# Optimization experiments

Hardware: AMD Instinct MI355X
Metric: run time of the kernel (lower is better)

The kernel has to match this reference:

```python
import jax, jax.numpy as jnp
import numpy as np

THRESHOLD = 0.5
NEG_POS = 3
ALPHA = 1.0


def cxcy_to_xy(b):
    return jnp.concatenate([b[:, :2] - b[:, 2:] / 2, b[:, :2] + b[:, 2:] / 2], axis=-1)


def xy_to_cxcy(b):
    return jnp.concatenate([(b[:, :2] + b[:, 2:]) / 2, b[:, 2:] - b[:, :2]], axis=-1)


def encode_bboxes(cxcy, priors_cxcy):
    # standard SSD encoding with variances (0.1, 0.2)
    g_cxcy = (cxcy[:, :2] - priors_cxcy[:, :2]) / (priors_cxcy[:, 2:] / 10.0)
    g_wh = jnp.log(cxcy[:, 2:] / priors_cxcy[:, 2:]) * 5.0
    return jnp.concatenate([g_cxcy, g_wh], axis=-1)


def compute_iou(a, b):
    # a: [n,4] xyxy, b: [m,4] xyxy -> [n,m]
    lt = jnp.maximum(a[:, None, :2], b[None, :, :2])
    rb = jnp.minimum(a[:, None, 2:], b[None, :, 2:])
    wh = jnp.clip(rb - lt, 0.0)
    inter = wh[..., 0] * wh[..., 1]
    area_a = (a[:, 2] - a[:, 0]) * (a[:, 3] - a[:, 1])
    area_b = (b[:, 2] - b[:, 0]) * (b[:, 3] - b[:, 1])
    return inter / (area_a[:, None] + area_b[None, :] - inter)


def setup_inputs() -> dict:
    key = jax.random.key(0)
    k1, k2, k3, k4, k5, k6 = jax.random.split(key, 6)
    B, D, C, O = 128, 8732, 21, 16
    loc_pred = jax.random.normal(k1, (B, D, 4), dtype=jnp.float32)
    cls_pred = jax.random.normal(k2, (B, D, C), dtype=jnp.float32)
    # valid gt boxes: xmin<xmax, ymin<ymax
    p = jax.random.uniform(k3, (B, O, 4), dtype=jnp.float32)
    x1 = jnp.minimum(p[..., 0], p[..., 2])
    x2 = jnp.maximum(p[..., 0], p[..., 2]) + 1e-2
    y1 = jnp.minimum(p[..., 1], p[..., 3])
    y2 = jnp.maximum(p[..., 1], p[..., 3]) + 1e-2
    gt_boxes = jnp.stack([x1, y1, x2, y2], axis=-1)
    gt_labels = jax.random.randint(k4, (B, O), 1, C)
    # priors in cxcywh, w/h in (0.05, 0.5)
    cxy = jax.random.uniform(k5, (D, 2), dtype=jnp.float32)
    wh = jax.random.uniform(k6, (D, 2), dtype=jnp.float32) * 0.45 + 0.05
    default_boxes = jnp.concatenate([cxy, wh], axis=-1)
    return {"loc_pred": loc_pred, "cls_pred": cls_pred, "gt_boxes": gt_boxes,
            "gt_labels": gt_labels, "default_boxes": default_boxes}


def _match_and_losses(loc_pred, cls_pred, gt_boxes, gt_labels, default_boxes):
    B, D, C = cls_pred.shape
    O = gt_boxes.shape[1]
    db_xy = cxcy_to_xy(default_boxes)

    def match_one(boxes_i, labels_i):
        iou = compute_iou(boxes_i, db_xy)                 # [O, D]
        best_truth_overlap = iou.max(axis=0)              # [D]
        best_truth_idx = iou.argmax(axis=0)               # [D]
        best_default_idx = iou.argmax(axis=1)             # [O]
        best_truth_idx = best_truth_idx.at[best_default_idx].set(jnp.arange(O))
        best_truth_overlap = best_truth_overlap.at[best_default_idx].set(1.0)
        labels = labels_i[best_truth_idx]                 # [D]
        labels = jnp.where(best_truth_overlap < THRESHOLD, 0, labels)
        matched_xy = boxes_i[best_truth_idx]              # [D,4]
        loc = encode_bboxes(xy_to_cxcy(matched_xy), default_boxes)
        return loc, labels

    loc_t, conf_t = jax.vmap(match_one)(gt_boxes, gt_labels)  # [B,D,4], [B,D]
    loc_t = jax.lax.stop_gradient(loc_t)  # targets carry no grad (requires_grad=False)

    pos = conf_t > 0                                      # [B,D]
    n_positive = pos.sum(axis=1)                          # [B]
    n_pos_total = n_positive.sum()

    # SmoothL1 (beta=1), mean over positive elements (num_pos * 4)
    diff = loc_pred - loc_t
    ad = jnp.abs(diff)
    sl1 = jnp.where(ad < 1.0, 0.5 * diff * diff, ad - 0.5)
    loc_loss = (sl1 * pos[..., None]).sum() / (n_pos_total.astype(jnp.float32) * 4.0)

    # per-element cross entropy
    logp = jax.nn.log_softmax(cls_pred, axis=-1)          # [B,D,C]
    ce = -jnp.take_along_axis(logp, conf_t[..., None], axis=-1)[..., 0]  # [B,D]

    conf_pos_sum = (ce * pos).sum()
    neg_loss = jnp.where(pos, 0.0, ce)
    neg_sorted = -jnp.sort(-neg_loss, axis=1)             # descending per row
    ranks = jnp.arange(D)[None, :]
    hard = ranks < (NEG_POS * n_positive)[:, None]
    conf_neg_sum = (neg_sorted * hard).sum()
    conf_loss = (conf_neg_sum + conf_pos_sum) / n_pos_total.astype(jnp.float32)

    return ALPHA * loc_loss + conf_loss


def reference(loc_pred, cls_pred, gt_boxes, gt_labels, default_boxes):
    return _match_and_losses(loc_pred, cls_pred, gt_boxes, gt_labels, default_boxes)
```

## Files before the change

kernel.cpp:

```cpp
#include <hip/hip_runtime.h>

#define BB 128
#define DD 8732
#define OO 16
#define CC 21
#define NG2 4366
#define NBLK_C 18
#define NLB (BB * NBLK_C)
#define NV 35

typedef float f32x2 __attribute__((ext_vector_type(2)));

__device__ __forceinline__ float smoothl1(float d) {
    float ad = fabsf(d);
    return (ad < 1.0f) ? 0.5f * d * d : ad - 0.5f;
}

__global__ __launch_bounds__(256) void fused_all(
    const float4* __restrict__ loc_pred,
    const float*  __restrict__ cls,
    const float4* __restrict__ gt_boxes,
    const int*    __restrict__ gt_labels,
    const float4* __restrict__ db,
    unsigned long long* __restrict__ partial,
    float* __restrict__ ce_neg,
    float* __restrict__ part_sl1,
    int*   __restrict__ part_np,
    float* __restrict__ part_ce)
{
    const int b = blockIdx.y, jb = blockIdx.x, tid = threadIdx.x;
    const int g = jb * 256 + tid;
    __shared__ float s_ax1[OO], s_ay1[OO], s_ax2[OO], s_ay2[OO], s_area[OO];
    __shared__ int   s_lab[OO];
    __shared__ unsigned long long s_keys[8][257];
    __shared__ float s_f[8];
    __shared__ int   s_i[4];

    if (tid < OO) {
        float4 gg = gt_boxes[b * OO + tid];
        s_ax1[tid] = gg.x; s_ay1[tid] = gg.y; s_ax2[tid] = gg.z; s_ay2[tid] = gg.w;
        s_area[tid] = (gg.z - gg.x) * (gg.w - gg.y);
        s_lab[tid] = gt_labels[b * OO + tid];
    }
    __syncthreads();

    unsigned long long key[OO];
    #pragma unroll
    for (int o = 0; o < OO; ++o) key[o] = 0ull;
    int lab_r[2] = {0, 0};
    int bi_r[2]  = {0, 0};

    const int row0 = g * 2;
    if (g < NG2) {
        #pragma unroll
        for (int r = 0; r < 2; ++r) {
            const int d = row0 + r;
            float4 p = db[d];
            float px1 = p.x - p.z * 0.5f, py1 = p.y - p.w * 0.5f;
            float px2 = p.x + p.z * 0.5f, py2 = p.y + p.w * 0.5f;
            float area_b = (px2 - px1) * (py2 - py1);
            unsigned dl = (unsigned)(DD - 1 - d);
            float best = -1.0f; int bi = 0;
            #pragma unroll
            for (int o = 0; o < OO; ++o) {
                float w = fmaxf(fminf(s_ax2[o], px2) - fmaxf(s_ax1[o], px1), 0.0f);
                float h = fmaxf(fminf(s_ay2[o], py2) - fmaxf(s_ay1[o], py1), 0.0f);
                float inter = w * h;
                float uni = s_area[o] + area_b - inter;
                float iou = inter * __builtin_amdgcn_rcpf(uni);
                unsigned long long kk = ((unsigned long long)__float_as_uint(iou) << 32) | dl;
                if (kk > key[o]) key[o] = kk;
                if (iou > best) { best = iou; bi = o; }
            }
            lab_r[r] = (best < 0.5f) ? 0 : s_lab[bi];
            bi_r[r]  = bi;
        }
    }

    #pragma unroll
    for (int o = 0; o < 8; ++o) s_keys[o][tid] = key[o];
    __syncthreads();
    if (tid < 128) {
        const int o = tid >> 4, j = tid & 15;
        unsigned long long mx = s_keys[o][j];
        #pragma unroll
        for (int m = 1; m < 16; ++m) {
            unsigned long long v = s_keys[o][j + 16 * m];
            if (v > mx) mx = v;
        }
        #pragma unroll
        for (int off = 8; off; off >>= 1) {
            unsigned long long v = __shfl_xor(mx, off, 16);
            if (v > mx) mx = v;
        }
        if (j == 0) atomicMax(&partial[b * OO + o], mx);
    }
    __syncthreads();
    #pragma unroll
    for (int o = 0; o < 8; ++o) s_keys[o][tid] = key[8 + o];
    __syncthreads();
    if (tid < 128) {
        const int o = tid >> 4, j = tid & 15;
        unsigned long long mx = s_keys[o][j];
        #pragma unroll
        for (int m = 1; m < 16; ++m) {
            unsigned long long v = s_keys[o][j + 16 * m];
            if (v > mx) mx = v;
        }
        #pragma unroll
        for (int off = 8; off; off >>= 1) {
            unsigned long long v = __shfl_xor(mx, off, 16);
            if (v > mx) mx = v;
        }
        if (j == 0) atomicMax(&partial[b * OO + 8 + o], mx);
    }

    float sl1 = 0.0f, cepos = 0.0f; int npos = 0;
    if (g < NG2) {
        const size_t gi2 = (size_t)b * DD + row0;
        float e[42];
        const f32x2* src = (const f32x2*)(cls + gi2 * CC);
        #pragma unroll
        for (int jv = 0; jv < 21; ++jv) {
            f32x2 q = src[jv];
            e[2*jv+0] = q[0]; e[2*jv+1] = q[1];
        }
        float out[2];
        #pragma unroll
        for (int r = 0; r < 2; ++r) {
            const int lab = lab_r[r];
            float m = e[21*r];
            #pragma unroll
            for (int c = 1; c < CC; ++c) m = fmaxf(m, e[21*r + c]);
            float s = 0.0f;
            #pragma unroll
            for (int c = 0; c < CC; ++c) s += __expf(e[21*r + c] - m);
            float xl = (lab == 0) ? e[21*r] : cls[(gi2 + r) * CC + lab];
            float ce = m + __logf(s) - xl;
            if (lab > 0) {
                npos += 1; cepos += ce;
                const int bi = bi_r[r];
                float ax1 = s_ax1[bi], ay1 = s_ay1[bi], ax2 = s_ax2[bi], ay2 = s_ay2[bi];
                float cx = (ax1 + ax2) * 0.5f, cy = (ay1 + ay2) * 0.5f;
                float w = ax2 - ax1, h = ay2 - ay1;
                float4 p = db[row0 + r];
                float gx = (cx - p.x) / (p.z / 10.0f);
                float gy = (cy - p.y) / (p.w / 10.0f);
                float gw = __logf(w / p.z) * 5.0f;
                float gh = __logf(h / p.w) * 5.0f;
                float4 lp = loc_pred[gi2 + r];
                sl1 += smoothl1(lp.x - gx) + smoothl1(lp.y - gy)
                     + smoothl1(lp.z - gw) + smoothl1(lp.w - gh);
                out[r] = 0.0f;
            } else {
                out[r] = ce;
            }
        }
        *(f32x2*)(ce_neg + gi2) = f32x2{out[0], out[1]};
    }

    #pragma unroll
    for (int off = 32; off; off >>= 1) {
        sl1   += __shfl_xor(sl1, off);
        cepos += __shfl_xor(cepos, off);
        npos  += __shfl_xor(npos, off);
    }
    const int w = tid >> 6;
    if ((tid & 63) == 0) { s_f[w*2+0] = sl1; s_f[w*2+1] = cepos; s_i[w] = npos; }
    __syncthreads();
    if (tid == 0) {
        float sv = 0, cp = 0; int np = 0;
        #pragma unroll
        for (int q = 0; q < 4; ++q) { sv += s_f[q*2+0]; cp += s_f[q*2+1]; np += s_i[q]; }
        const int pi = b * NBLK_C + jb;
        part_sl1[pi] = sv;
        part_ce[pi]  = cp;
        part_np[pi]  = np;
    }
}

__global__ __launch_bounds__(256) void topk_final(
    const float*  __restrict__ cls,
    const float4* __restrict__ loc_pred,
    const float4* __restrict__ gt_boxes,
    const int*    __restrict__ gt_labels,
    const float4* __restrict__ db,
    const unsigned long long* __restrict__ partial,
    float* __restrict__ ce_neg,
    const float* __restrict__ part_sl1,
    const int*   __restrict__ part_np,
    const float* __restrict__ part_ce,
    float* __restrict__ img_sl1,
    float* __restrict__ img_ce,
    int*   __restrict__ img_np,
    float* __restrict__ conf_neg_part,
    int*   __restrict__ done_counter,
    float* __restrict__ out)
{
    const int b = blockIdx.x, tid = threadIdx.x;
    __shared__ int      hist[256];
    __shared__ unsigned s_pk[2];
    __shared__ float    s_f[12];
    __shared__ int      s_c[4];
    __shared__ int      s_bdi[OO], s_lab[OO];
    __shared__ float    s_ax1[OO], s_ay1[OO], s_ax2[OO], s_ay2[OO], s_area[OO];
    __shared__ float    s_dsl1, s_dce;
    __shared__ int      s_dnp, s_np;
    __shared__ float    s_isl1, s_ice;
    __shared__ int      s_last;

    if (tid < OO) {
        float4 gg = gt_boxes[b * OO + tid];
        s_ax1[tid] = gg.x; s_ay1[tid] = gg.y; s_ax2[tid] = gg.z; s_ay2[tid] = gg.w;
        s_area[tid] = (gg.z - gg.x) * (gg.w - gg.y);
        s_lab[tid] = gt_labels[b * OO + tid];
        s_bdi[tid] = DD - 1 - (int)(partial[b * OO + tid] & 0xffffffffu);
    }
    __syncthreads();

    float dsl1 = 0.0f, dce = 0.0f; int dnp = 0;
    if (tid < OO) {
        const int R = s_bdi[tid];
        bool winner = true;
        for (int o2 = tid + 1; o2 < OO; ++o2)
            if (s_bdi[o2] == R) winner = false;
        if (winner) {
            float4 p = db[R];
            float px1 = p.x - p.z * 0.5f, py1 = p.y - p.w * 0.5f;
            float px2 = p.x + p.z * 0.5f, py2 = p.y + p.w * 0.5f;
            float area_b = (px2 - px1) * (py2 - py1);
            float best = -1.0f; int bi = 0;
            #pragma unroll
            for (int o = 0; o < OO; ++o) {
                float w = fmaxf(fminf(s_ax2[o], px2) - fmaxf(s_ax1[o], px1), 0.0f);
                float h = fmaxf(fminf(s_ay2[o], py2) - fmaxf(s_ay1[o], py1), 0.0f);
                float inter = w * h;
                float uni = s_area[o] + area_b - inter;
                float iou = inter * __builtin_amdgcn_rcpf(uni);
                if (iou > best) { best = iou; bi = o; }
            }
            int lab0 = (best < 0.5f) ? 0 : s_lab[bi];

            const float* x = cls + ((size_t)b * DD + R) * CC;
            float m = x[0];
            #pragma unroll
            for (int c = 1; c < CC; ++c) m = fmaxf(m, x[c]);
            float s = 0.0f;
            #pragma unroll
            for (int c = 0; c < CC; ++c) s += __expf(x[c] - m);
            float lse = m + __logf(s);
            float4 lp = loc_pred[(size_t)b * DD + R];

            if (lab0 > 0) {
                dce -= (lse - x[lab0]);
                dnp -= 1;
                float ax1 = s_ax1[bi], ay1 = s_ay1[bi], ax2 = s_ax2[bi], ay2 = s_ay2[bi];
                float cx = (ax1 + ax2) * 0.5f, cy = (ay1 + ay2) * 0.5f;
                float w = ax2 - ax1, h = ay2 - ay1;
                float gx = (cx - p.x) / (p.z / 10.0f);
                float gy = (cy - p.y) / (p.w / 10.0f);
                float gw = __logf(w / p.z) * 5.0f;
                float gh = __logf(h / p.w) * 5.0f;
                dsl1 -= smoothl1(lp.x - gx) + smoothl1(lp.y - gy)
                      + smoothl1(lp.z - gw) + smoothl1(lp.w - gh);
            } else {
                ce_neg[(size_t)b * DD + R] = 0.0f;
            }
            dce += (lse - x[s_lab[tid]]);
            dnp += 1;
            {
                float ax1 = s_ax1[tid], ay1 = s_ay1[tid], ax2 = s_ax2[tid], ay2 = s_ay2[tid];
                float cx = (ax1 + ax2) * 0.5f, cy = (ay1 + ay2) * 0.5f;
                float w = ax2 - ax1, h = ay2 - ay1;
                float gx = (cx - p.x) / (p.z / 10.0f);
                float gy = (cy - p.y) / (p.w / 10.0f);
                float gw = __logf(w / p.z) * 5.0f;
                float gh = __logf(h / p.w) * 5.0f;
                dsl1 += smoothl1(lp.x - gx) + smoothl1(lp.y - gy)
                      + smoothl1(lp.z - gw) + smoothl1(lp.w - gh);
            }
        }
    }
    if (tid < 64) {
        #pragma unroll
        for (int off = 8; off; off >>= 1) {
            dsl1 += __shfl_xor(dsl1, off, 16);
            dce  += __shfl_xor(dce, off, 16);
            dnp  += __shfl_xor(dnp, off, 16);
        }
        if (tid == 0) { s_dsl1 = dsl1; s_dce = dce; s_dnp = dnp; }
    }
    __syncthreads();

    if (tid == 0) {
        float a = 0, c2 = 0; int n = 0;
        #pragma unroll
        for (int j = 0; j < NBLK_C; ++j) {
            a  += part_sl1[b * NBLK_C + j];
            c2 += part_ce[b * NBLK_C + j];
            n  += part_np[b * NBLK_C + j];
        }
        s_isl1 = a + s_dsl1; s_ice = c2 + s_dce; s_np = n + s_dnp;
    }
    __syncthreads();

    int k0 = 3 * s_np;
    if (k0 > DD) k0 = DD;

    float row = 0.0f;
    if (k0 > 0) {
        unsigned kx[NV];
        #pragma unroll
        for (int q = 0; q < NV; ++q) {
            int d = q * 256 + tid;
            float v = (d < DD) ? ce_neg[(size_t)b * DD + d] : 0.0f;
            unsigned u = __float_as_uint(v);
            kx[q] = u ^ ((unsigned)((int)u >> 31) | 0x80000000u);
        }
        unsigned prefix = 0u; int k = k0;
        #pragma unroll
        for (int p = 0; p < 4; ++p) {
            const int shift = 24 - 8 * p;
            hist[tid] = 0;
            __syncthreads();
            #pragma unroll
            for (int q = 0; q < NV; ++q) {
                if (p == 0 || ((kx[q] ^ prefix) >> (shift + 8)) == 0u)
                    atomicAdd(&hist[(kx[q] >> shift) & 255], 1);
            }
            __syncthreads();
            if (tid < 64) {
                int h0 = hist[255 - 4*tid], h1 = hist[254 - 4*tid],
                    h2 = hist[253 - 4*tid], h3 = hist[252 - 4*tid];
                int sl = h0 + h1 + h2 + h3;
                int run = sl;
                #pragma unroll
                for (int off = 1; off < 64; off <<= 1) {
                    int v = __shfl_up(run, off);
                    if (tid >= off) run += v;
                }
                int pre = run - sl;
                if (pre < k && k <= pre + sl) {
                    int hh[4] = {h0, h1, h2, h3};
                    int c = pre, byte = -1, knew = 0;
                    #pragma unroll
                    for (int j = 0; j < 4; ++j) {
                        if (byte < 0 && c + hh[j] >= k) { byte = 255 - 4*tid - j; knew = k - c; }
                        c += hh[j];
                    }
                    s_pk[0] = prefix | ((unsigned)byte << shift);
                    s_pk[1] = (unsigned)knew;
                }
            }
            __syncthreads();
            prefix = s_pk[0]; k = (int)s_pk[1];
        }
        unsigned vb = (prefix & 0x80000000u) ? (prefix ^ 0x80000000u) : ~prefix;
        float vk = __uint_as_float(vb);

        float ssum = 0.0f; int cgt = 0;
        #pragma unroll
        for (int q = 0; q < NV; ++q) {
            if (kx[q] > prefix) {
                unsigned u = (kx[q] & 0x80000000u) ? (kx[q] ^ 0x80000000u) : ~kx[q];
                ssum += __uint_as_float(u);
                ++cgt;
            }
        }
        #pragma unroll
        for (int off = 32; off; off >>= 1) { ssum += __shfl_xor(ssum, off); cgt += __shfl_xor(cgt, off); }
        if ((tid & 63) == 0) { s_f[tid >> 6] = ssum; s_c[tid >> 6] = cgt; }
        __syncthreads();
        row = s_f[0]+s_f[1]+s_f[2]+s_f[3]
            + (float)(k0 - (s_c[0]+s_c[1]+s_c[2]+s_c[3])) * vk;
    }

    if (tid == 0) {
        conf_neg_part[b] = row;
        img_sl1[b] = s_isl1; img_ce[b] = s_ice; img_np[b] = s_np;
        __threadfence();
        int prev = atomicAdd(done_counter, 1);
        s_last = (prev == BB - 1) ? 1 : 0;
    }
    __syncthreads();
    if (s_last) {
        __threadfence();
        float loc = 0.0f, cp = 0.0f, cn = 0.0f; int npt = 0;
        if (tid < BB) {
            loc = img_sl1[tid]; cp = img_ce[tid];
            cn = conf_neg_part[tid]; npt = img_np[tid];
        }
        #pragma unroll
        for (int off = 32; off; off >>= 1) {
            loc += __shfl_xor(loc, off);
            cp  += __shfl_xor(cp, off);
            cn  += __shfl_xor(cn, off);
            npt += __shfl_xor(npt, off);
        }
        const int w = tid >> 6;
        if ((tid & 63) == 0) { s_f[w*3+0] = loc; s_f[w*3+1] = cp; s_f[w*3+2] = cn; s_c[w] = npt; }
        __syncthreads();
        if (tid == 0) {
            float L = 0, P = 0, N = 0; int T = 0;
            #pragma unroll
            for (int q = 0; q < 4; ++q) { L += s_f[q*3]; P += s_f[q*3+1]; N += s_f[q*3+2]; T += s_c[q]; }
            float npf = (float)T;
            out[0] = L / (npf * 4.0f) + (N + P) / npf;
        }
    }
}

extern "C" void kernel_launch(void* const* d_in, const int* in_sizes, int n_in,
                              void* d_out, int out_size, void* d_ws, size_t ws_size,
                              hipStream_t stream) {
    (void)in_sizes; (void)n_in; (void)out_size; (void)ws_size;
    const float4* loc_pred  = (const float4*)d_in[0];
    const float*  cls_pred  = (const float*)d_in[1];
    const float4* gt_boxes  = (const float4*)d_in[2];
    const int*    gt_labels = (const int*)d_in[3];
    const float4* db        = (const float4*)d_in[4];

    char* ws = (char*)d_ws;
    size_t off = 0;
    auto alloc = [&](size_t bytes) { char* p = ws + off; off = (off + bytes + 15) & ~(size_t)15; return p; };

    unsigned long long* partial = (unsigned long long*)alloc((size_t)BB * OO * 8);
    int*   done_counter  = (int*)alloc(16);
    float* ce_neg        = (float*)alloc((size_t)BB * DD * 4);
    float* part_sl1      = (float*)alloc((size_t)NLB * 4);
    int*   part_np       = (int*)alloc((size_t)NLB * 4);
    float* part_ce       = (float*)alloc((size_t)NLB * 4);
    float* img_sl1       = (float*)alloc((size_t)BB * 4);
    float* img_ce        = (float*)alloc((size_t)BB * 4);
    int*   img_np        = (int*)alloc((size_t)BB * 4);
    float* conf_neg_part = (float*)alloc((size_t)BB * 4);

    hipMemsetAsync(partial, 0, (size_t)BB * OO * 8 + 16, stream);

    fused_all<<<dim3(NBLK_C, BB), 256, 0, stream>>>(loc_pred, cls_pred, gt_boxes,
                                                    gt_labels, db, partial,
                                                    ce_neg, part_sl1, part_np, part_ce);
    topk_final<<<BB, 256, 0, stream>>>(cls_pred, loc_pred, gt_boxes, gt_labels, db,
                                       partial, ce_neg, part_sl1, part_np, part_ce,
                                       img_sl1, img_ce, img_np, conf_neg_part,
                                       done_counter, (float*)d_out);
}
```

Before: 60.05 us.

## Pack IoU/index keys into 32 bits, reduce via wave shuffles, prefetch logits

The per-ground-truth best-prior key becomes a 32-bit value: the IoU's upper bits are packed with a 14-bit inverted prior index. The cross-thread max then uses wave-level shuffles and a tiny per-wave shared array instead of two passes through a large 64-bit LDS buffer with extra barriers. The class-logit loads are moved ahead of the IoU loop so their memory latency can overlap the matching arithmetic. Truncating the IoU mantissa can change which prior is chosen when IoUs are nearly equal. Holding the loaded logits across the IoU loop also raises register pressure.

```diff
diff --git a/kernel.cpp b/kernel.cpp
--- a/kernel.cpp
+++ b/kernel.cpp
@@ -22,7 +22,7 @@
     const float4* __restrict__ gt_boxes,
     const int*    __restrict__ gt_labels,
     const float4* __restrict__ db,
-    unsigned long long* __restrict__ partial,
+    unsigned* __restrict__ partial,
     float* __restrict__ ce_neg,
     float* __restrict__ part_sl1,
     int*   __restrict__ part_np,
@@ -32,7 +32,7 @@
     const int g = jb * 256 + tid;
     __shared__ float s_ax1[OO], s_ay1[OO], s_ax2[OO], s_ay2[OO], s_area[OO];
     __shared__ int   s_lab[OO];
-    __shared__ unsigned long long s_keys[8][257];
+    __shared__ unsigned swave[4][OO];
     __shared__ float s_f[8];
     __shared__ int   s_i[4];
 
@@ -44,13 +44,25 @@
     }
     __syncthreads();
 
-    unsigned long long key[OO];
+    const int row0 = g * 2;
+    const size_t gi2 = (size_t)b * DD + row0;
+
+    float e[42];
+    if (g < NG2) {
+        const f32x2* src = (const f32x2*)(cls + gi2 * CC);
+        #pragma unroll
+        for (int jv = 0; jv < 21; ++jv) {
+            f32x2 q = src[jv];
+            e[2*jv+0] = q[0]; e[2*jv+1] = q[1];
+        }
+    }
+
+    unsigned key[OO];
     #pragma unroll
-    for (int o = 0; o < OO; ++o) key[o] = 0ull;
+    for (int o = 0; o < OO; ++o) key[o] = 0u;
     int lab_r[2] = {0, 0};
     int bi_r[2]  = {0, 0};
 
-    const int row0 = g * 2;
     if (g < NG2) {
         #pragma unroll
         for (int r = 0; r < 2; ++r) {
@@ -59,7 +71,7 @@
             float px1 = p.x - p.z * 0.5f, py1 = p.y - p.w * 0.5f;
             float px2 = p.x + p.z * 0.5f, py2 = p.y + p.w * 0.5f;
             float area_b = (px2 - px1) * (py2 - py1);
-            unsigned dl = (unsigned)(DD - 1 - d);
+            const unsigned dl = (unsigned)(16383 - d);
             float best = -1.0f; int bi = 0;
             #pragma unroll
             for (int o = 0; o < OO; ++o) {
@@ -68,7 +80,7 @@
                 float inter = w * h;
                 float uni = s_area[o] + area_b - inter;
                 float iou = inter * __builtin_amdgcn_rcpf(uni);
-                unsigned long long kk = ((unsigned long long)__float_as_uint(iou) << 32) | dl;
+                unsigned kk = (__float_as_uint(iou) & 0xFFFFC000u) | dl;
                 if (kk > key[o]) key[o] = kk;
                 if (iou > best) { best = iou; bi = o; }
             }
@@ -78,53 +90,25 @@
     }
 
     #pragma unroll
-    for (int o = 0; o < 8; ++o) s_keys[o][tid] = key[o];
-    __syncthreads();
-    if (tid < 128) {
-        const int o = tid >> 4, j = tid & 15;
-        unsigned long long mx = s_keys[o][j];
-        #pragma unroll
-        for (int m = 1; m < 16; ++m) {
-            unsigned long long v = s_keys[o][j + 16 * m];
-            if (v > mx) mx = v;
-        }
-        #pragma unroll
-        for (int off = 8; off; off >>= 1) {
-            unsigned long long v = __shfl_xor(mx, off, 16);
-            if (v > mx) mx = v;
-        }
-        if (j == 0) atomicMax(&partial[b * OO + o], mx);
-    }
-    __syncthreads();
-    #pragma unroll
-    for (int o = 0; o < 8; ++o) s_keys[o][tid] = key[8 + o];
-    __syncthreads();
-    if (tid < 128) {
-        const int o = tid >> 4, j = tid & 15;
-        unsigned long long mx = s_keys[o][j];
-        #pragma unroll
-        for (int m = 1; m < 16; ++m) {
-            unsigned long long v = s_keys[o][j + 16 * m];
-            if (v > mx) mx = v;
-        }
-        #pragma unroll
-        for (int off = 8; off; off >>= 1) {
-            unsigned long long v = __shfl_xor(mx, off, 16);
-            if (v > mx) mx = v;
-        }
-        if (j == 0) atomicMax(&partial[b * OO + 8 + o], mx);
+    for (int o = 0; o < OO; ++o) {
+        unsigned k = key[o];
+        #pragma unroll
+        for (int off = 32; off; off >>= 1) {
+            unsigned v = __shfl_xor(k, off);
+            if (v > k) k = v;
+        }
+        if ((tid & 63) == 0) swave[tid >> 6][o] = k;
+    }
+    __syncthreads();
+    if (tid < OO) {
+        unsigned m = swave[0][tid];
+        #pragma unroll
+        for (int w = 1; w < 4; ++w) if (swave[w][tid] > m) m = swave[w][tid];
+        atomicMax(&partial[b * OO + tid], m);
     }
 
     float sl1 = 0.0f, cepos = 0.0f; int npos = 0;
     if (g < NG2) {
-        const size_t gi2 = (size_t)b * DD + row0;
-        float e[42];
-        const f32x2* src = (const f32x2*)(cls + gi2 * CC);
-        #pragma unroll
-        for (int jv = 0; jv < 21; ++jv) {
-            f32x2 q = src[jv];
-            e[2*jv+0] = q[0]; e[2*jv+1] = q[1];
-        }
         float out[2];
         #pragma unroll
         for (int r = 0; r < 2; ++r) {
@@ -185,7 +169,7 @@
     const float4* __restrict__ gt_boxes,
     const int*    __restrict__ gt_labels,
     const float4* __restrict__ db,
-    const unsigned long long* __restrict__ partial,
+    const unsigned* __restrict__ partial,
     float* __restrict__ ce_neg,
     const float* __restrict__ part_sl1,
     const int*   __restrict__ part_np,
@@ -214,7 +198,7 @@
         s_ax1[tid] = gg.x; s_ay1[tid] = gg.y; s_ax2[tid] = gg.z; s_ay2[tid] = gg.w;
         s_area[tid] = (gg.z - gg.x) * (gg.w - gg.y);
         s_lab[tid] = gt_labels[b * OO + tid];
-        s_bdi[tid] = DD - 1 - (int)(partial[b * OO + tid] & 0xffffffffu);
+        s_bdi[tid] = 16383 - (int)(partial[b * OO + tid] & 0x3FFFu);
     }
     __syncthreads();
 
@@ -424,7 +408,7 @@
     size_t off = 0;
     auto alloc = [&](size_t bytes) { char* p = ws + off; off = (off + bytes + 15) & ~(size_t)15; return p; };
 
-    unsigned long long* partial = (unsigned long long*)alloc((size_t)BB * OO * 8);
+    unsigned* partial    = (unsigned*)alloc((size_t)BB * OO * 4);
     int*   done_counter  = (int*)alloc(16);
     float* ce_neg        = (float*)alloc((size_t)BB * DD * 4);
     float* part_sl1      = (float*)alloc((size_t)NLB * 4);
@@ -435,7 +419,7 @@
     int*   img_np        = (int*)alloc((size_t)BB * 4);
     float* conf_neg_part = (float*)alloc((size_t)BB * 4);
 
-    hipMemsetAsync(partial, 0, (size_t)BB * OO * 8 + 16, stream);
+    hipMemsetAsync(partial, 0, (size_t)BB * OO * 4 + 16, stream);
 
     fused_all<<<dim3(NBLK_C, BB), 256, 0, stream>>>(loc_pred, cls_pred, gt_boxes,
                                                     gt_labels, db, partial,
```

Result: slower. 67.09 us (+11.7%).
